# Kernel optimization log

Measured on AMD Instinct MI355X. Metric: run time of the kernel, lower is better.

The kernel has to match this reference:

```python
import jax, jax.numpy as jnp
import numpy as np
import math

HIDDEN = 1024
HEADS = 16
D_K = HIDDEN // HEADS
B, S = 2, 2048


def setup_inputs() -> dict:
    key = jax.random.key(0)
    ks = jax.random.split(key, 12)
    sc = 1.0 / math.sqrt(HIDDEN)
    inp = {
        "q": jax.random.normal(ks[0], (B, S, HIDDEN), jnp.float32),
        "k": jax.random.normal(ks[1], (B, S, HIDDEN), jnp.float32),
        "v": jax.random.normal(ks[2], (B, S, HIDDEN), jnp.float32),
        "mask": jax.random.randint(ks[3], (B, 1, S, S), 0, 2, jnp.int32),
        "Wq": jax.random.normal(ks[4], (HIDDEN, HIDDEN), jnp.float32) * sc,
        "bq": jnp.zeros((HIDDEN,), jnp.float32),
        "Wk": jax.random.normal(ks[5], (HIDDEN, HIDDEN), jnp.float32) * sc,
        "bk": jnp.zeros((HIDDEN,), jnp.float32),
        "Wv": jax.random.normal(ks[6], (HIDDEN, HIDDEN), jnp.float32) * sc,
        "bv": jnp.zeros((HIDDEN,), jnp.float32),
        "Wo": jax.random.normal(ks[7], (HIDDEN, HIDDEN), jnp.float32) * sc,
        "bo": jnp.zeros((HIDDEN,), jnp.float32),
    }
    return inp


def reference(q, k, v, mask, Wq, bq, Wk, bk, Wv, bv, Wo, bo):
    bs, sq, _ = q.shape
    # project and split heads: [b, h, s, d_k]
    qh = (q @ Wq + bq).reshape(bs, sq, HEADS, D_K).transpose(0, 2, 1, 3)
    kh = (k @ Wk + bk).reshape(bs, -1, HEADS, D_K).transpose(0, 2, 1, 3)
    vh = (v @ Wv + bv).reshape(bs, -1, HEADS, D_K).transpose(0, 2, 1, 3)
    scores = jnp.einsum("bhqd,bhkd->bhqk", qh, kh) / math.sqrt(D_K)
    scores = jnp.where(mask == 0, -jnp.inf, scores)
    attn = jax.nn.softmax(scores, axis=-1)
    attn = jnp.nan_to_num(attn, nan=0.0)  # dropout is identity in eval
    x = jnp.einsum("bhqk,bhkd->bhqd", attn, vh)
    x = x.transpose(0, 2, 1, 3).reshape(bs, sq, HIDDEN)
    return x @ Wo + bo
```

## Files before the change

kernel.cpp:

```cpp
#include <hip/hip_runtime.h>
#include <hip/hip_bf16.h>
#include <math.h>

#define HIDDEN 1024
#define HEADS 16
#define DK 64
#define BATCH 2
#define SLEN 2048

typedef __attribute__((ext_vector_type(8))) short short8v;
typedef __attribute__((ext_vector_type(4))) float f32x4;

__device__ __forceinline__ float bf_f(unsigned short h) {
  unsigned u = ((unsigned)h) << 16;
  return __builtin_bit_cast(float, u);
}
__device__ __forceinline__ void split_t(float x, unsigned short& hi,
                                        unsigned short& lo) {
  unsigned xu = __builtin_bit_cast(unsigned, x);
  float r = x - __builtin_bit_cast(float, xu & 0xffff0000u);
  hi = (unsigned short)(xu >> 16);
  lo = (unsigned short)(__builtin_bit_cast(unsigned, r) >> 16);
}
__device__ __forceinline__ unsigned pack_hl_t(float x) {
  unsigned xu = __builtin_bit_cast(unsigned, x);
  float r = x - __builtin_bit_cast(float, xu & 0xffff0000u);
  unsigned ru = __builtin_bit_cast(unsigned, r);
  return __builtin_amdgcn_perm(ru, xu, 0x07060302u);
}

__device__ __forceinline__ short8v unpack8(const uint4& a0, const uint4& a1,
                                           unsigned sel) {
  uint4 r;
  r.x = __builtin_amdgcn_perm(a0.y, a0.x, sel);
  r.y = __builtin_amdgcn_perm(a0.w, a0.z, sel);
  r.z = __builtin_amdgcn_perm(a1.y, a1.x, sel);
  r.w = __builtin_amdgcn_perm(a1.w, a1.z, sel);
  return __builtin_bit_cast(short8v, r);
}
#define SEL_HI 0x05040100u
#define SEL_LO 0x07060302u

#define GLB_US(p) ((const __attribute__((address_space(1))) unsigned short*)(p))
#define LDS_US(p) ((__attribute__((address_space(3))) unsigned short*)(p))

#define QSCALE 0.18033688011112042f

__global__ __launch_bounds__(256) void mask_bits_kernel(
    const int* __restrict__ mask, unsigned long long* __restrict__ Mb)
{
  const int row = blockIdx.x * 4 + (threadIdx.x >> 6);
  const int lane = threadIdx.x & 63;
  const int* mr = mask + (size_t)row * SLEN;
#pragma unroll
  for (int t = 0; t < 32; ++t) {
    int m = mr[t * 64 + lane];
    unsigned long long bits = __ballot(m != 0);
    if (lane == 0) Mb[(size_t)row * 32 + t] = bits;
  }
}

__global__ __launch_bounds__(256) void pack_act_kernel(
    const float* __restrict__ src, unsigned short* __restrict__ hi,
    unsigned short* __restrict__ lo, int n4)
{
  int stride = gridDim.x * blockDim.x;
  for (int i = blockIdx.x * blockDim.x + threadIdx.x; i < n4; i += stride) {
    float4 v = ((const float4*)src)[i];
    ushort4 H, L;
    split_t(v.x, H.x, L.x); split_t(v.y, H.y, L.y);
    split_t(v.z, H.z, L.z); split_t(v.w, H.w, L.w);
    *(ushort4*)(hi + (size_t)i * 4) = H;
    *(ushort4*)(lo + (size_t)i * 4) = L;
  }
}

__global__ __launch_bounds__(256) void pack_wT_kernel(
    const float* __restrict__ W, unsigned short* __restrict__ Whi,
    unsigned short* __restrict__ Wlo)
{
  __shared__ float T[64][65];
  const int t = threadIdx.x;
  const int bk = blockIdx.x >> 4, bn = blockIdx.x & 15;
#pragma unroll
  for (int i = 0; i < 4; ++i) {
    int k = (t >> 4) + i * 16, n = (t & 15) * 4;
    float4 v = *(const float4*)(W + (size_t)(bk * 64 + k) * HIDDEN + bn * 64 + n);
    T[k][n + 0] = v.x; T[k][n + 1] = v.y; T[k][n + 2] = v.z; T[k][n + 3] = v.w;
  }
  __syncthreads();
  const int nl = t & 63, kc = (t >> 6) * 16;
#pragma unroll
  for (int i = 0; i < 4; ++i) {
    ushort4 H, L;
    split_t(T[kc + i * 4 + 0][nl], H.x, L.x);
    split_t(T[kc + i * 4 + 1][nl], H.y, L.y);
    split_t(T[kc + i * 4 + 2][nl], H.z, L.z);
    split_t(T[kc + i * 4 + 3][nl], H.w, L.w);
    size_t base = (size_t)(bn * 64 + nl) * HIDDEN + bk * 64 + kc + i * 4;
    *(ushort4*)(Whi + base) = H;
    *(ushort4*)(Wlo + base) = L;
  }
}

__global__ __launch_bounds__(256) void gemm_sp_kernel(
    const unsigned short* __restrict__ Ahi, const unsigned short* __restrict__ Alo,
    const unsigned short* __restrict__ Bthi, const unsigned short* __restrict__ Btlo,
    const float* __restrict__ bias, float oscale,
    unsigned short* __restrict__ Yhi, unsigned short* __restrict__ Ylo,
    float* __restrict__ Yf, int mode)
{
  __shared__ __align__(16) unsigned short lds[2][4][64 * 32];

  const int tid = threadIdx.x;
  const int xcd = blockIdx.x & 7;
  const int idx = blockIdx.x >> 3;
  const int bm = xcd * 8 + (idx & 7);
  const int bn = idx >> 3;
  const int m0 = bm * 64, n0 = bn * 64;
  const int w = tid >> 6, lane = tid & 63;
  const int wm = w >> 1, wn = w & 1;
  const int g = lane >> 4, qi = lane & 15;

  const int tr = tid >> 2;
  const int tc = (((tid & 3) ^ ((tid >> 3) & 3)) << 3);
  const int dofs = tid * 8;

  f32x4 acc[2][2];
#pragma unroll
  for (int mt = 0; mt < 2; ++mt)
#pragma unroll
    for (int nt = 0; nt < 2; ++nt) acc[mt][nt] = (f32x4){0.f, 0.f, 0.f, 0.f};

  auto stage = [&](int buf, int k0) {
    size_t ga = (size_t)(m0 + tr) * HIDDEN + k0 + tc;
    size_t gb = (size_t)(n0 + tr) * HIDDEN + k0 + tc;
    __builtin_amdgcn_global_load_lds(GLB_US(Ahi + ga), LDS_US(&lds[buf][0][dofs]), 16, 0, 0);
    __builtin_amdgcn_global_load_lds(GLB_US(Alo + ga), LDS_US(&lds[buf][1][dofs]), 16, 0, 0);
    __builtin_amdgcn_global_load_lds(GLB_US(Bthi + gb), LDS_US(&lds[buf][2][dofs]), 16, 0, 0);
    __builtin_amdgcn_global_load_lds(GLB_US(Btlo + gb), LDS_US(&lds[buf][3][dofs]), 16, 0, 0);
  };

  auto compute = [&](int buf) {
    short8v a_h[2], a_l[2], b_h[2], b_l[2];
#pragma unroll
    for (int mt = 0; mt < 2; ++mt) {
      int R = wm * 32 + mt * 16 + qi;
      int cofs = R * 32 + ((g ^ ((R >> 1) & 3)) << 3);
      a_h[mt] = *(const short8v*)&lds[buf][0][cofs];
      a_l[mt] = *(const short8v*)&lds[buf][1][cofs];
    }
#pragma unroll
    for (int nt = 0; nt < 2; ++nt) {
      int R = wn * 32 + nt * 16 + qi;
      int cofs = R * 32 + ((g ^ ((R >> 1) & 3)) << 3);
      b_h[nt] = *(const short8v*)&lds[buf][2][cofs];
      b_l[nt] = *(const short8v*)&lds[buf][3][cofs];
    }
#pragma unroll
    for (int nt = 0; nt < 2; ++nt)
#pragma unroll
      for (int mt = 0; mt < 2; ++mt) {
        acc[mt][nt] = __builtin_amdgcn_mfma_f32_16x16x32_bf16(a_h[mt], b_h[nt], acc[mt][nt], 0, 0, 0);
        acc[mt][nt] = __builtin_amdgcn_mfma_f32_16x16x32_bf16(a_l[mt], b_h[nt], acc[mt][nt], 0, 0, 0);
        acc[mt][nt] = __builtin_amdgcn_mfma_f32_16x16x32_bf16(a_h[mt], b_l[nt], acc[mt][nt], 0, 0, 0);
      }
  };

  stage(0, 0);
  __syncthreads();
  for (int t = 0; t < 31; ++t) {
    stage((t + 1) & 1, (t + 1) * 32);
    compute(t & 1);
    __syncthreads();
  }
  compute(1);

#pragma unroll
  for (int nt = 0; nt < 2; ++nt) {
    int n = n0 + wn * 32 + nt * 16 + qi;
    float bv = bias[n];
#pragma unroll
    for (int mt = 0; mt < 2; ++mt) {
#pragma unroll
      for (int r = 0; r < 4; ++r) {
        int m = m0 + wm * 32 + mt * 16 + g * 4 + r;
        float val = (acc[mt][nt][r] + bv) * oscale;
        if (mode == 0) {
          Yf[(size_t)m * HIDDEN + n] = val;
        } else {
          int s = m & (SLEN - 1);
          int bh_ = (m >> 11) * HEADS + (n >> 6);
          int d = n & 63;
          unsigned short hi, lo;
          split_t(val, hi, lo);
          size_t base = (mode == 1) ? (((size_t)bh_ * SLEN + s) << 6) + d
                                    : ((size_t)(bh_ * DK + d)) * SLEN + s;
          Yhi[base] = hi;
          Ylo[base] = lo;
        }
      }
    }
  }
}

__global__ __launch_bounds__(512) void attn_mfma_kernel(
    const unsigned short* __restrict__ Qhi, const unsigned short* __restrict__ Qlo,
    const unsigned short* __restrict__ Khi, const unsigned short* __restrict__ Klo,
    const unsigned short* __restrict__ Vthi, const unsigned short* __restrict__ Vtlo,
    const unsigned long long* __restrict__ Mb,
    unsigned short* __restrict__ XaHi, unsigned short* __restrict__ XaLo)
{
  __shared__ __align__(16) unsigned char smem[49152];
  unsigned short* Ks_hi = (unsigned short*)smem;
  unsigned short* Ks_lo = (unsigned short*)(smem + 8192);
  unsigned short* Vs_hi = (unsigned short*)(smem + 16384);
  unsigned short* Vs_lo = (unsigned short*)(smem + 24576);

  const int tid = threadIdx.x;
  const int bx = blockIdx.x;
  const int lb = (bx & 7) * 64 + (bx >> 3);
  const int qt = lb & 15;
  const int bh = lb >> 4;
  const int b = bh >> 4, h = bh & 15;
  const int w = tid >> 6, lane = tid & 63;
  const int g = lane >> 4, qi = lane & 15;
  const int qbase = qt * 128 + w * 16;

  unsigned* Pw = (unsigned*)(w < 4 ? (smem + w * 4096)
                                   : (smem + 32768 + (w - 4) * 4096));

  short8v qh[2], ql[2];
  {
    const unsigned short* qr_hi = Qhi + ((size_t)bh * SLEN + qbase + qi) * DK;
    const unsigned short* qr_lo = Qlo + ((size_t)bh * SLEN + qbase + qi) * DK;
    qh[0] = *(const short8v*)(qr_hi + g * 8);
    qh[1] = *(const short8v*)(qr_hi + 32 + g * 8);
    ql[0] = *(const short8v*)(qr_lo + g * 8);
    ql[1] = *(const short8v*)(qr_lo + 32 + g * 8);
  }

  f32x4 o[4];
#pragma unroll
  for (int dt = 0; dt < 4; ++dt) o[dt] = (f32x4){0.f, 0.f, 0.f, 0.f};
  float m_run = -1e30f, l_run = 0.f;

  const unsigned long long* mrow = Mb + ((size_t)b * SLEN + qbase + qi) * 32;

  const int srow = tid >> 3;
  const int scol = (((tid & 7) ^ (srow & 7)) << 3);
  const int sdof = tid * 8;

  for (int k0 = 0; k0 < SLEN; k0 += 64) {
    __syncthreads();
    {
      size_t gk = ((size_t)bh * SLEN + k0 + srow) * 64 + scol;
      size_t gv = ((size_t)(bh * 64 + srow)) * SLEN + k0 + scol;
      __builtin_amdgcn_global_load_lds(GLB_US(Khi + gk), LDS_US(Ks_hi + sdof), 16, 0, 0);
      __builtin_amdgcn_global_load_lds(GLB_US(Klo + gk), LDS_US(Ks_lo + sdof), 16, 0, 0);
      __builtin_amdgcn_global_load_lds(GLB_US(Vthi + gv), LDS_US(Vs_hi + sdof), 16, 0, 0);
      __builtin_amdgcn_global_load_lds(GLB_US(Vtlo + gv), LDS_US(Vs_lo + sdof), 16, 0, 0);
    }
    __syncthreads();

    f32x4 sf[4];
#pragma unroll
    for (int ks = 0; ks < 4; ++ks) {
      int krow = ks * 16 + qi;
      int cswz = (krow & 7) << 3;
      short8v kh0 = *(const short8v*)&Ks_hi[krow * 64 + ((g * 8) ^ cswz)];
      short8v kh1 = *(const short8v*)&Ks_hi[krow * 64 + ((32 + g * 8) ^ cswz)];
      short8v kl0 = *(const short8v*)&Ks_lo[krow * 64 + ((g * 8) ^ cswz)];
      short8v kl1 = *(const short8v*)&Ks_lo[krow * 64 + ((32 + g * 8) ^ cswz)];
      f32x4 s = {0.f, 0.f, 0.f, 0.f};
      s = __builtin_amdgcn_mfma_f32_16x16x32_bf16(kh0, qh[0], s, 0, 0, 0);
      s = __builtin_amdgcn_mfma_f32_16x16x32_bf16(kh1, qh[1], s, 0, 0, 0);
      s = __builtin_amdgcn_mfma_f32_16x16x32_bf16(kh0, ql[0], s, 0, 0, 0);
      s = __builtin_amdgcn_mfma_f32_16x16x32_bf16(kh1, ql[1], s, 0, 0, 0);
      s = __builtin_amdgcn_mfma_f32_16x16x32_bf16(kl0, qh[0], s, 0, 0, 0);
      s = __builtin_amdgcn_mfma_f32_16x16x32_bf16(kl1, qh[1], s, 0, 0, 0);
      sf[ks] = s;
    }
    __syncthreads();

    unsigned long long mw = mrow[k0 >> 6];
    unsigned s0 = ((unsigned)mw) >> (g * 4);
    unsigned s1 = ((unsigned)(mw >> 32)) >> (g * 4);
    float sv[4][4];
    float rowmax = -INFINITY;
#pragma unroll
    for (int ks = 0; ks < 4; ++ks) {
      unsigned sel = (ks < 2) ? s0 : s1;
#pragma unroll
      for (int r = 0; r < 4; ++r) {
        float x = sf[ks][r];
        sv[ks][r] = ((sel >> (((ks & 1) << 4) + r)) & 1) ? x : -INFINITY;
        rowmax = fmaxf(rowmax, sv[ks][r]);
      }
    }
    rowmax = fmaxf(rowmax, __shfl_xor(rowmax, 16));
    rowmax = fmaxf(rowmax, __shfl_xor(rowmax, 32));

    if (__any(rowmax > m_run + 11.5f)) {
      float mnew = fmaxf(m_run, rowmax);
      float scale = exp2f(m_run - mnew);
      l_run *= scale;
#pragma unroll
      for (int r = 0; r < 4; ++r) {
        float sc = __shfl(scale, g * 4 + r);
        o[0][r] *= sc; o[1][r] *= sc; o[2][r] *= sc; o[3][r] *= sc;
      }
      m_run = mnew;
    }

    float lsum = 0.f;
#pragma unroll
    for (int ks = 0; ks < 4; ++ks)
#pragma unroll
      for (int r = 0; r < 4; ++r) {
        float pv = exp2f(sv[ks][r] - m_run);
        lsum += pv;
        int k = ks * 16 + g * 4 + r;
        int wa = (k << 4) + qi;
        wa ^= ((wa >> 7) & 1) << 4;
        Pw[wa] = pack_hl_t(pv);
      }
    lsum += __shfl_xor(lsum, 16);
    lsum += __shfl_xor(lsum, 32);
    l_run += lsum;

#pragma unroll
    for (int kh = 0; kh < 2; ++kh) {
      unsigned u0, u1, u2, u3, u4, u5, u6, u7;
      {
        int kb = kh * 32 + g * 8;
        int ra;
        ra = ((kb + 0) << 4) + qi; ra ^= ((ra >> 7) & 1) << 4; u0 = Pw[ra];
        ra = ((kb + 1) << 4) + qi; ra ^= ((ra >> 7) & 1) << 4; u1 = Pw[ra];
        ra = ((kb + 2) << 4) + qi; ra ^= ((ra >> 7) & 1) << 4; u2 = Pw[ra];
        ra = ((kb + 3) << 4) + qi; ra ^= ((ra >> 7) & 1) << 4; u3 = Pw[ra];
        ra = ((kb + 4) << 4) + qi; ra ^= ((ra >> 7) & 1) << 4; u4 = Pw[ra];
        ra = ((kb + 5) << 4) + qi; ra ^= ((ra >> 7) & 1) << 4; u5 = Pw[ra];
        ra = ((kb + 6) << 4) + qi; ra ^= ((ra >> 7) & 1) << 4; u6 = Pw[ra];
        ra = ((kb + 7) << 4) + qi; ra ^= ((ra >> 7) & 1) << 4; u7 = Pw[ra];
      }
      uint4 a0 = {u0, u1, u2, u3}, a1 = {u4, u5, u6, u7};
      short8v phi = unpack8(a0, a1, SEL_HI);
      short8v plo = unpack8(a0, a1, SEL_LO);
#pragma unroll
      for (int dt = 0; dt < 4; ++dt) {
        int drow = dt * 16 + qi;
        int vcol = (kh * 32 + g * 8) ^ ((drow & 7) << 3);
        short8v vh = *(const short8v*)&Vs_hi[drow * 64 + vcol];
        short8v vl = *(const short8v*)&Vs_lo[drow * 64 + vcol];
        o[dt] = __builtin_amdgcn_mfma_f32_16x16x32_bf16(phi, vh, o[dt], 0, 0, 0);
        o[dt] = __builtin_amdgcn_mfma_f32_16x16x32_bf16(phi, vl, o[dt], 0, 0, 0);
        o[dt] = __builtin_amdgcn_mfma_f32_16x16x32_bf16(plo, vh, o[dt], 0, 0, 0);
      }
    }
  }

#pragma unroll
  for (int r = 0; r < 4; ++r) {
    float lr = __shfl(l_run, g * 4 + r);
    float inv = lr > 0.f ? 1.f / lr : 0.f;
    size_t rowa = ((size_t)(b * SLEN) + qbase + g * 4 + r) * HIDDEN + h * DK;
#pragma unroll
    for (int dt = 0; dt < 4; ++dt) {
      float val = o[dt][r] * inv;
      unsigned short hi, lo;
      split_t(val, hi, lo);
      XaHi[rowa + dt * 16 + qi] = hi;
      XaLo[rowa + dt * 16 + qi] = lo;
    }
  }
}

extern "C" void kernel_launch(void* const* d_in, const int* in_sizes, int n_in,
                              void* d_out, int out_size, void* d_ws, size_t ws_size,
                              hipStream_t stream) {
  const float* q   = (const float*)d_in[0];
  const float* k   = (const float*)d_in[1];
  const float* v   = (const float*)d_in[2];
  const int*  mask = (const int*)d_in[3];
  const float* Wq  = (const float*)d_in[4];
  const float* bq  = (const float*)d_in[5];
  const float* Wk  = (const float*)d_in[6];
  const float* bk  = (const float*)d_in[7];
  const float* Wv  = (const float*)d_in[8];
  const float* bv  = (const float*)d_in[9];
  const float* Wo  = (const float*)d_in[10];
  const float* bo  = (const float*)d_in[11];
  float* out = (float*)d_out;

  const size_t HSZ = (size_t)BATCH * SLEN * HIDDEN;
  const size_t WSZ = (size_t)HIDDEN * HIDDEN;
  unsigned short* wsu = (unsigned short*)d_ws;
  unsigned short* Qhi = wsu;
  unsigned short* Qlo = wsu + HSZ;
  unsigned short* Khi = wsu + 2 * HSZ;
  unsigned short* Klo = wsu + 3 * HSZ;
  unsigned short* Vthi = wsu + 4 * HSZ;
  unsigned short* Vtlo = wsu + 5 * HSZ;
  unsigned short* Ahi_ = wsu + 6 * HSZ;
  unsigned short* Alo_ = wsu + 7 * HSZ;
  unsigned short* Wthi = wsu + 8 * HSZ;
  unsigned short* Wtlo = wsu + 8 * HSZ + WSZ;
  unsigned long long* Mb = (unsigned long long*)(wsu + 8 * HSZ + 2 * WSZ);

  const int n4 = (int)(HSZ / 4);

  mask_bits_kernel<<<BATCH * SLEN / 4, 256, 0, stream>>>(mask, Mb);

  pack_act_kernel<<<1024, 256, 0, stream>>>(q, Ahi_, Alo_, n4);
  pack_wT_kernel<<<256, 256, 0, stream>>>(Wq, Wthi, Wtlo);
  gemm_sp_kernel<<<1024, 256, 0, stream>>>(Ahi_, Alo_, Wthi, Wtlo, bq, QSCALE, Qhi, Qlo, nullptr, 1);
  pack_act_kernel<<<1024, 256, 0, stream>>>(k, Ahi_, Alo_, n4);
  pack_wT_kernel<<<256, 256, 0, stream>>>(Wk, Wthi, Wtlo);
  gemm_sp_kernel<<<1024, 256, 0, stream>>>(Ahi_, Alo_, Wthi, Wtlo, bk, 1.0f, Khi, Klo, nullptr, 1);
  pack_act_kernel<<<1024, 256, 0, stream>>>(v, Ahi_, Alo_, n4);
  pack_wT_kernel<<<256, 256, 0, stream>>>(Wv, Wthi, Wtlo);
  gemm_sp_kernel<<<1024, 256, 0, stream>>>(Ahi_, Alo_, Wthi, Wtlo, bv, 1.0f, Vthi, Vtlo, nullptr, 2);

  attn_mfma_kernel<<<512, 512, 0, stream>>>(Qhi, Qlo, Khi, Klo, Vthi, Vtlo,
                                            Mb, Ahi_, Alo_);

  pack_wT_kernel<<<256, 256, 0, stream>>>(Wo, Wthi, Wtlo);
  gemm_sp_kernel<<<1024, 256, 0, stream>>>(Ahi_, Alo_, Wthi, Wtlo, bo, 1.0f, nullptr, nullptr, out, 0);
}
```

Measured before the change: 468.5 us.

## Enlarge GEMM tiles to 128x128 and raise wave priority around attention MFMAs

The split-bf16 projection GEMM moves from 64x64 to 128x128 output tiles, so each wave computes a 4x4 grid of MFMA tiles and the grid shrinks from 1024 to 256 blocks with a new XCD-aware block mapping. The goal is more operand reuse per LDS load and fewer global loads per FLOP. The cost is higher register pressure, double the LDS footprint, and only 256 blocks, which may underfill the 256 CUs. Separately, the attention kernel wraps its MFMA sections in s_setprio so waves issuing matrix work get scheduling priority over waves doing softmax.

```diff
diff --git a/kernel.cpp b/kernel.cpp
--- a/kernel.cpp
+++ b/kernel.cpp
@@ -110,57 +110,59 @@
     unsigned short* __restrict__ Yhi, unsigned short* __restrict__ Ylo,
     float* __restrict__ Yf, int mode)
 {
-  __shared__ __align__(16) unsigned short lds[2][4][64 * 32];
+  __shared__ __align__(16) unsigned short lds[2][4][128 * 32];
 
   const int tid = threadIdx.x;
-  const int xcd = blockIdx.x & 7;
-  const int idx = blockIdx.x >> 3;
-  const int bm = xcd * 8 + (idx & 7);
-  const int bn = idx >> 3;
-  const int m0 = bm * 64, n0 = bn * 64;
+  const int lb = (blockIdx.x & 7) * 32 + (blockIdx.x >> 3);
+  const int bm = lb >> 3;
+  const int bn = lb & 7;
+  const int m0 = bm * 128, n0 = bn * 128;
   const int w = tid >> 6, lane = tid & 63;
   const int wm = w >> 1, wn = w & 1;
   const int g = lane >> 4, qi = lane & 15;
 
-  const int tr = tid >> 2;
-  const int tc = (((tid & 3) ^ ((tid >> 3) & 3)) << 3);
-  const int dofs = tid * 8;
-
-  f32x4 acc[2][2];
-#pragma unroll
-  for (int mt = 0; mt < 2; ++mt)
-#pragma unroll
-    for (int nt = 0; nt < 2; ++nt) acc[mt][nt] = (f32x4){0.f, 0.f, 0.f, 0.f};
+  f32x4 acc[4][4];
+#pragma unroll
+  for (int mt = 0; mt < 4; ++mt)
+#pragma unroll
+    for (int nt = 0; nt < 4; ++nt) acc[mt][nt] = (f32x4){0.f, 0.f, 0.f, 0.f};
 
   auto stage = [&](int buf, int k0) {
-    size_t ga = (size_t)(m0 + tr) * HIDDEN + k0 + tc;
-    size_t gb = (size_t)(n0 + tr) * HIDDEN + k0 + tc;
-    __builtin_amdgcn_global_load_lds(GLB_US(Ahi + ga), LDS_US(&lds[buf][0][dofs]), 16, 0, 0);
-    __builtin_amdgcn_global_load_lds(GLB_US(Alo + ga), LDS_US(&lds[buf][1][dofs]), 16, 0, 0);
-    __builtin_amdgcn_global_load_lds(GLB_US(Bthi + gb), LDS_US(&lds[buf][2][dofs]), 16, 0, 0);
-    __builtin_amdgcn_global_load_lds(GLB_US(Btlo + gb), LDS_US(&lds[buf][3][dofs]), 16, 0, 0);
+#pragma unroll
+    for (int i = 0; i < 2; ++i) {
+      int c = tid + i * 256;
+      int r = c >> 2;
+      int tc = (((c & 3) ^ ((r >> 1) & 3)) << 3);
+      size_t ga = (size_t)(m0 + r) * HIDDEN + k0 + tc;
+      size_t gb = (size_t)(n0 + r) * HIDDEN + k0 + tc;
+      int d = c * 8;
+      __builtin_amdgcn_global_load_lds(GLB_US(Ahi + ga), LDS_US(&lds[buf][0][d]), 16, 0, 0);
+      __builtin_amdgcn_global_load_lds(GLB_US(Alo + ga), LDS_US(&lds[buf][1][d]), 16, 0, 0);
+      __builtin_amdgcn_global_load_lds(GLB_US(Bthi + gb), LDS_US(&lds[buf][2][d]), 16, 0, 0);
+      __builtin_amdgcn_global_load_lds(GLB_US(Btlo + gb), LDS_US(&lds[buf][3][d]), 16, 0, 0);
+    }
   };
 
   auto compute = [&](int buf) {
-    short8v a_h[2], a_l[2], b_h[2], b_l[2];
-#pragma unroll
-    for (int mt = 0; mt < 2; ++mt) {
-      int R = wm * 32 + mt * 16 + qi;
+    short8v a_h[4], a_l[4], b_h[4], b_l[4];
+#pragma unroll
+    for (int mt = 0; mt < 4; ++mt) {
+      int R = wm * 64 + mt * 16 + qi;
       int cofs = R * 32 + ((g ^ ((R >> 1) & 3)) << 3);
       a_h[mt] = *(const short8v*)&lds[buf][0][cofs];
       a_l[mt] = *(const short8v*)&lds[buf][1][cofs];
     }
 #pragma unroll
-    for (int nt = 0; nt < 2; ++nt) {
-      int R = wn * 32 + nt * 16 + qi;
+    for (int nt = 0; nt < 4; ++nt) {
+      int R = wn * 64 + nt * 16 + qi;
       int cofs = R * 32 + ((g ^ ((R >> 1) & 3)) << 3);
       b_h[nt] = *(const short8v*)&lds[buf][2][cofs];
       b_l[nt] = *(const short8v*)&lds[buf][3][cofs];
     }
 #pragma unroll
-    for (int nt = 0; nt < 2; ++nt)
-#pragma unroll
-      for (int mt = 0; mt < 2; ++mt) {
+    for (int nt = 0; nt < 4; ++nt)
+#pragma unroll
+      for (int mt = 0; mt < 4; ++mt) {
         acc[mt][nt] = __builtin_amdgcn_mfma_f32_16x16x32_bf16(a_h[mt], b_h[nt], acc[mt][nt], 0, 0, 0);
         acc[mt][nt] = __builtin_amdgcn_mfma_f32_16x16x32_bf16(a_l[mt], b_h[nt], acc[mt][nt], 0, 0, 0);
         acc[mt][nt] = __builtin_amdgcn_mfma_f32_16x16x32_bf16(a_h[mt], b_l[nt], acc[mt][nt], 0, 0, 0);
@@ -177,14 +179,14 @@
   compute(1);
 
 #pragma unroll
-  for (int nt = 0; nt < 2; ++nt) {
-    int n = n0 + wn * 32 + nt * 16 + qi;
+  for (int nt = 0; nt < 4; ++nt) {
+    int n = n0 + wn * 64 + nt * 16 + qi;
     float bv = bias[n];
 #pragma unroll
-    for (int mt = 0; mt < 2; ++mt) {
+    for (int mt = 0; mt < 4; ++mt) {
 #pragma unroll
       for (int r = 0; r < 4; ++r) {
-        int m = m0 + wm * 32 + mt * 16 + g * 4 + r;
+        int m = m0 + wm * 64 + mt * 16 + g * 4 + r;
         float val = (acc[mt][nt][r] + bv) * oscale;
         if (mode == 0) {
           Yf[(size_t)m * HIDDEN + n] = val;
@@ -264,6 +266,7 @@
     __syncthreads();
 
     f32x4 sf[4];
+    __builtin_amdgcn_s_setprio(1);
 #pragma unroll
     for (int ks = 0; ks < 4; ++ks) {
       int krow = ks * 16 + qi;
@@ -281,6 +284,7 @@
       s = __builtin_amdgcn_mfma_f32_16x16x32_bf16(kl1, qh[1], s, 0, 0, 0);
       sf[ks] = s;
     }
+    __builtin_amdgcn_s_setprio(0);
     __syncthreads();
 
     unsigned long long mw = mrow[k0 >> 6];
@@ -347,6 +351,7 @@
       uint4 a0 = {u0, u1, u2, u3}, a1 = {u4, u5, u6, u7};
       short8v phi = unpack8(a0, a1, SEL_HI);
       short8v plo = unpack8(a0, a1, SEL_LO);
+      __builtin_amdgcn_s_setprio(1);
 #pragma unroll
       for (int dt = 0; dt < 4; ++dt) {
         int drow = dt * 16 + qi;
@@ -357,6 +362,7 @@
         o[dt] = __builtin_amdgcn_mfma_f32_16x16x32_bf16(phi, vl, o[dt], 0, 0, 0);
         o[dt] = __builtin_amdgcn_mfma_f32_16x16x32_bf16(plo, vh, o[dt], 0, 0, 0);
       }
+      __builtin_amdgcn_s_setprio(0);
     }
   }
 
@@ -414,17 +420,17 @@
 
   pack_act_kernel<<<1024, 256, 0, stream>>>(q, Ahi_, Alo_, n4);
   pack_wT_kernel<<<256, 256, 0, stream>>>(Wq, Wthi, Wtlo);
-  gemm_sp_kernel<<<1024, 256, 0, stream>>>(Ahi_, Alo_, Wthi, Wtlo, bq, QSCALE, Qhi, Qlo, nullptr, 1);
+  gemm_sp_kernel<<<256, 256, 0, stream>>>(Ahi_, Alo_, Wthi, Wtlo, bq, QSCALE, Qhi, Qlo, nullptr, 1);
   pack_act_kernel<<<1024, 256, 0, stream>>>(k, Ahi_, Alo_, n4);
   pack_wT_kernel<<<256, 256, 0, stream>>>(Wk, Wthi, Wtlo);
-  gemm_sp_kernel<<<1024, 256, 0, stream>>>(Ahi_, Alo_, Wthi, Wtlo, bk, 1.0f, Khi, Klo, nullptr, 1);
+  gemm_sp_kernel<<<256, 256, 0, stream>>>(Ahi_, Alo_, Wthi, Wtlo, bk, 1.0f, Khi, Klo, nullptr, 1);
   pack_act_kernel<<<1024, 256, 0, stream>>>(v, Ahi_, Alo_, n4);
   pack_wT_kernel<<<256, 256, 0, stream>>>(Wv, Wthi, Wtlo);
-  gemm_sp_kernel<<<1024, 256, 0, stream>>>(Ahi_, Alo_, Wthi, Wtlo, bv, 1.0f, Vthi, Vtlo, nullptr, 2);
+  gemm_sp_kernel<<<256, 256, 0, stream>>>(Ahi_, Alo_, Wthi, Wtlo, bv, 1.0f, Vthi, Vtlo, nullptr, 2);
 
   attn_mfma_kernel<<<512, 512, 0, stream>>>(Qhi, Qlo, Khi, Klo, Vthi, Vtlo,
                                             Mb, Ahi_, Alo_);
 
   pack_wT_kernel<<<256, 256, 0, stream>>>(Wo, Wthi, Wtlo);
-  gemm_sp_kernel<<<1024, 256, 0, stream>>>(Ahi_, Alo_, Wthi, Wtlo, bo, 1.0f, nullptr, nullptr, out, 0);
-}
+  gemm_sp_kernel<<<256, 256, 0, stream>>>(Ahi_, Alo_, Wthi, Wtlo, bo, 1.0f, nullptr, nullptr, out, 0);
+}
```

Measured after the change: 457.4 us. 2.4% less time.
